# Optimization experiments

Measured on AMD Instinct MI355X. Metric: run time of the kernel, lower is better.

Reference implementation:

```python
import jax, jax.numpy as jnp
import numpy as np

# ---- dims / hyperparams (match init_kwargs) ----
D, B, S, NE, NC = 256, 4, 8192, 2048, 512
WIN, RK, TKE, TKC = 4, 4, 4, 4          # s window, route_topk, expanded_topk, compressed_topk
ALPHA, BS2B, BB2S = 1.0, 0.5, 0.5       # alpha_b, beta_s_to_b, beta_b_to_s
S_SC, B_SC, X_SC = 0.25, 0.2, 0.15      # s/b/cross delta scales
EPS = 1e-5
INV_SQRT_D = float(1.0 / np.sqrt(D))


def _ln(x, g, b):
    m = jnp.mean(x, -1, keepdims=True)
    v = jnp.mean(jnp.square(x - m), -1, keepdims=True)
    return (x - m) * jax.lax.rsqrt(v + EPS) * g + b


def _window_prop(state, val, w):
    # local window attention via diagonal-bilinear pairwise scores; never builds [S,S]
    n = state.shape[1]
    offs = jnp.arange(-WIN, WIN + 1)
    idx = jnp.arange(n)[:, None] + offs[None, :]            # [n, K]
    valid = (idx >= 0) & (idx < n)
    idxc = jnp.clip(idx, 0, n - 1)
    nb_s = state[:, idxc]                                    # [B, n, K, D]
    nb_v = val[:, idxc]
    sc = jnp.einsum('bnd,bnkd->bnk', state * w, nb_s) * INV_SQRT_D
    sc = jnp.where(valid, sc, -1e30)
    a = jax.nn.softmax(sc, axis=-1)
    return (jnp.einsum('bnk,bnkd->bnd', a, nb_s),
            jnp.einsum('bnk,bnkd->bnd', a, nb_v))


def _topk_prop(state, val, w, k):
    # global topk sparse attention over the (small) expanded/compressed node set
    sc = jnp.einsum('bnd,bmd->bnm', state * w, state) * INV_SQRT_D
    top, idx = jax.lax.top_k(sc, k)                          # [B, N, k]
    a = jax.nn.softmax(top, axis=-1)
    take = jax.vmap(lambda x, i: x[i])                       # gather rows per batch
    nb_s = take(state, idx)                                  # [B, N, k, D]
    nb_v = take(val, idx)
    return (jnp.einsum('bnk,bnkd->bnd', a, nb_s),
            jnp.einsum('bnk,bnkd->bnd', a, nb_v))


def _sparse_transition(src_s, src_v, W, bias, nd, k):
    # LinearRoute logits -> topk dst per src -> softmax weights -> scatter-add into dst
    logits = src_s @ W + bias                                # [B, Ns, Nd]
    top, idx = jax.lax.top_k(logits, k)
    wgt = jax.nn.softmax(top, axis=-1)                       # [B, Ns, k]

    def scat(i, ww, fs, fv):
        ii = i.reshape(-1)
        cs = (ww[..., None] * fs[:, None, :]).reshape(-1, fs.shape[-1])
        cv = (ww[..., None] * fv[:, None, :]).reshape(-1, fv.shape[-1])
        z = jnp.zeros((nd, fs.shape[-1]), fs.dtype)
        return z.at[ii].add(cs), z.at[ii].add(cv)

    return jax.vmap(scat)(idx, wgt, src_s, src_v)            # [B, Nd, D] x2


def _forward(s_state, s_val, w_pair_s, w_pair_e, w_pair_c,
             W_expand, b_expand, W_b2s, b_b2s, W_comp, b_comp, W_s2b, b_s2b,
             ln_g_s, ln_b_s, ln_g_e, ln_b_e, ln_g_c, ln_b_c):
    bsz = s_state.shape[0]
    # 1) sequence window propagation + stabilize
    ds, dv = _window_prop(s_state, s_val, w_pair_s)
    s_state = jnp.tanh(s_state + S_SC * ds)
    s_val = _ln(s_val + S_SC * dv, ln_g_s, ln_b_s)
    # 2) compressed layer bootstrapped from zeros (compressed_b=None) + stabilize
    c_state = jnp.zeros((bsz, NC, D), s_state.dtype)
    c_val = _ln(jnp.zeros((bsz, NC, D), s_state.dtype), ln_g_c, ln_b_c)
    # 3) expanded layer: expand transition then topk propagation + stabilize
    e_state = jnp.zeros((bsz, NE, D), s_state.dtype)
    e_val = jnp.zeros((bsz, NE, D), s_state.dtype)
    sc_b = ALPHA * B_SC
    ds, dv = _sparse_transition(c_state, c_val, W_expand, b_expand, NE, RK)
    e_state = e_state + sc_b * ds; e_val = e_val + sc_b * dv
    ds, dv = _topk_prop(e_state, e_val, w_pair_e, TKE)
    e_state = jnp.tanh(e_state + sc_b * ds)
    e_val = _ln(e_val + sc_b * dv, ln_g_e, ln_b_e)
    # 4) expanded -> sequence cross update + stabilize
    sc_x = ALPHA * BB2S * X_SC
    ds, dv = _sparse_transition(e_state, e_val, W_b2s, b_b2s, S, RK)
    s_state = jnp.tanh(s_state + sc_x * ds)
    s_val = _ln(s_val + sc_x * dv, ln_g_s, ln_b_s)
    # 5) next compressed: compress, s->b, compressed propagation + stabilize
    nc_state, nc_val = c_state, c_val
    ds, dv = _sparse_transition(e_state, e_val, W_comp, b_comp, NC, RK)
    nc_state = nc_state + sc_b * ds; nc_val = nc_val + sc_b * dv
    sc_sb = ALPHA * BS2B * X_SC
    ds, dv = _sparse_transition(s_state, s_val, W_s2b, b_s2b, NC, RK)
    nc_state = nc_state + sc_sb * ds; nc_val = nc_val + sc_sb * dv
    ds, dv = _topk_prop(nc_state, nc_val, w_pair_c, TKC)
    nc_state = jnp.tanh(nc_state + sc_b * ds)
    nc_val = _ln(nc_val + sc_b * dv, ln_g_c, ln_b_c)
    return (s_state, s_val, nc_state, nc_val)


def setup_inputs() -> dict:
    key = jax.random.key(0)
    ks = jax.random.split(key, 16)
    rs = float(1.0 / np.sqrt(D))
    return {
        's_state': jax.random.normal(ks[0], (B, S, D), jnp.float32),
        's_val': jax.random.normal(ks[1], (B, S, D), jnp.float32),
        'w_pair_s': jax.random.normal(ks[2], (D,), jnp.float32) * rs,
        'w_pair_e': jax.random.normal(ks[3], (D,), jnp.float32) * rs,
        'w_pair_c': jax.random.normal(ks[4], (D,), jnp.float32) * rs,
        'W_expand': jax.random.normal(ks[5], (D, NE), jnp.float32) * rs,
        'b_expand': jnp.zeros((NE,), jnp.float32),
        'W_b2s': jax.random.normal(ks[6], (D, S), jnp.float32) * rs,
        'b_b2s': jnp.zeros((S,), jnp.float32),
        'W_comp': jax.random.normal(ks[7], (D, NC), jnp.float32) * rs,
        'b_comp': jnp.zeros((NC,), jnp.float32),
        'W_s2b': jax.random.normal(ks[8], (D, NC), jnp.float32) * rs,
        'b_s2b': jnp.zeros((NC,), jnp.float32),
        'ln_g_s': jnp.ones((D,), jnp.float32), 'ln_b_s': jnp.zeros((D,), jnp.float32),
        'ln_g_e': jnp.ones((D,), jnp.float32), 'ln_b_e': jnp.zeros((D,), jnp.float32),
        'ln_g_c': jnp.ones((D,), jnp.float32), 'ln_b_c': jnp.zeros((D,), jnp.float32),
    }


def reference(s_state, s_val, w_pair_s, w_pair_e, w_pair_c,
              W_expand, b_expand, W_b2s, b_b2s, W_comp, b_comp, W_s2b, b_s2b,
              ln_g_s, ln_b_s, ln_g_e, ln_b_e, ln_g_c, ln_b_c):
    return _forward(s_state, s_val, w_pair_s, w_pair_e, w_pair_c,
                    W_expand, b_expand, W_b2s, b_b2s, W_comp, b_comp, W_s2b, b_s2b,
                    ln_g_s, ln_b_s, ln_g_e, ln_b_e, ln_g_c, ln_b_c)
```

## Files before the change

kernel.cpp:

```cpp
#include <hip/hip_runtime.h>
#include <math.h>

#define DD 256
#define BATCH 4
#define SEQ 8192
#define NEE 2048
#define NCC 512
#define EPSL 1e-5f
#define INV_SQRT_D 0.0625f

typedef __attribute__((ext_vector_type(8))) short short8;
typedef __attribute__((ext_vector_type(4))) float f32x4;

__device__ __forceinline__ float4 ld4(const float* p){ return *(const float4*)p; }
__device__ __forceinline__ void st4(float* p, const float4& v){ *(float4*)p = v; }
__device__ __forceinline__ void fma4(float4& a, float s, const float4& b){
  a.x = fmaf(s,b.x,a.x); a.y = fmaf(s,b.y,a.y); a.z = fmaf(s,b.z,a.z); a.w = fmaf(s,b.w,a.w);
}
__device__ __forceinline__ float4 tanh4(const float4& v){
  float4 r; r.x=tanhf(v.x); r.y=tanhf(v.y); r.z=tanhf(v.z); r.w=tanhf(v.w); return r;
}
__device__ __forceinline__ ushort f2bf(float x){
  unsigned u = __float_as_uint(x);
  unsigned r = u + 0x7fffu + ((u >> 16) & 1u);
  return (ushort)(r >> 16);
}
__device__ __forceinline__ float bf2f(ushort h){
  return __uint_as_float(((unsigned)h) << 16);
}

__device__ __forceinline__ bool t4_better(float v1, int i1, float v2, int i2){
  return (v1 > v2) || (v1 == v2 && i1 < i2);
}
__device__ __forceinline__ void t4_init(float* v, int* i){
#pragma unroll
  for (int k=0;k<4;k++){ v[k] = -INFINITY; i[k] = 0x7fffffff; }
}
__device__ __forceinline__ void t4_insert(float* v, int* i, float nv, int ni){
  if (t4_better(nv, ni, v[3], i[3])){
    v[3]=nv; i[3]=ni;
    if (t4_better(v[3],i[3],v[2],i[2])){ float tv=v[2]; v[2]=v[3]; v[3]=tv; int ti=i[2]; i[2]=i[3]; i[3]=ti;
      if (t4_better(v[2],i[2],v[1],i[1])){ tv=v[1]; v[1]=v[2]; v[2]=tv; ti=i[1]; i[1]=i[2]; i[2]=ti;
        if (t4_better(v[1],i[1],v[0],i[0])){ tv=v[0]; v[0]=v[1]; v[1]=tv; ti=i[0]; i[0]=i[1]; i[1]=ti; }
      }
    }
  }
}
__device__ __forceinline__ void t4_ce(float* v, int* i, int x, int y){
  if (t4_better(v[y],i[y],v[x],i[x])){ float tv=v[x]; v[x]=v[y]; v[y]=tv; int ti=i[x]; i[x]=i[y]; i[y]=ti; }
}
__device__ __forceinline__ void t4_merge(float* av, int* ai, const float* bv, const int* bi){
  float lv[4]; int li[4];
#pragma unroll
  for (int k=0;k<4;k++){
    if (t4_better(av[k],ai[k],bv[3-k],bi[3-k])){ lv[k]=av[k]; li[k]=ai[k]; }
    else { lv[k]=bv[3-k]; li[k]=bi[3-k]; }
  }
  t4_ce(lv,li,0,2); t4_ce(lv,li,1,3); t4_ce(lv,li,0,1); t4_ce(lv,li,2,3);
#pragma unroll
  for (int k=0;k<4;k++){ av[k]=lv[k]; ai[k]=li[k]; }
}
__device__ __forceinline__ void t4_wave_merge(float* v, int* i){
#pragma unroll
  for (int off=1; off<64; off<<=1){
    float bv[4]; int bi[4];
#pragma unroll
    for (int k=0;k<4;k++){ bv[k]=__shfl_xor(v[k],off); bi[k]=__shfl_xor(i[k],off); }
    t4_merge(v,i,bv,bi);
  }
}

__global__ __launch_bounds__(1024) void k0_prep(
    const float* __restrict__ b_expand, const float* __restrict__ b_b2s, const float* __restrict__ b_comp,
    const float* __restrict__ ln_b_c, const float* __restrict__ ln_g_e, const float* __restrict__ ln_b_e,
    float* __restrict__ sumE, int* __restrict__ idxB2S, float* __restrict__ wgtB2S,
    int* __restrict__ idxComp, float* __restrict__ wgtComp)
{
  __shared__ float wv_v[16][4];
  __shared__ int   wv_i[16][4];
  __shared__ int s_idx[3][4];
  __shared__ float s_wgt[3][4];
  __shared__ float red[16];
  int t = threadIdx.x, wv = t>>6, lane = t&63;
  {
    const float* arr; int n, base_wv, nw;
    if (wv < 2){ arr = b_expand; n = NEE; base_wv = 0;  nw = 2; }
    else if (wv < 14){ arr = b_b2s; n = SEQ; base_wv = 2; nw = 12; }
    else { arr = b_comp; n = NCC; base_wv = 14; nw = 2; }
    int gl = ((wv - base_wv)<<6) + lane;
    int stride = nw<<6;
    float v[4]; int ix[4]; t4_init(v,ix);
    for (int m=gl; m<n; m+=stride) t4_insert(v,ix, arr[m], m);
    t4_wave_merge(v,ix);
    if (lane==0){
#pragma unroll
      for (int k=0;k<4;k++){ wv_v[wv][k]=v[k]; wv_i[wv][k]=ix[k]; }
    }
  }
  __syncthreads();
  if (t < 3){
    int b0 = (t==0)? 0 : (t==1? 2 : 14);
    int nwv = (t==0)? 2 : (t==1? 12 : 2);
    float v[4]; int ix[4]; t4_init(v,ix);
    for (int wq=b0; wq<b0+nwv; wq++)
#pragma unroll
      for (int k=0;k<4;k++) t4_insert(v,ix, wv_v[wq][k], wv_i[wq][k]);
    float e0=1.f, e1=expf(v[1]-v[0]), e2=expf(v[2]-v[0]), e3=expf(v[3]-v[0]);
    float inv = 1.f/(e0+e1+e2+e3);
    s_idx[t][0]=ix[0]; s_idx[t][1]=ix[1]; s_idx[t][2]=ix[2]; s_idx[t][3]=ix[3];
    s_wgt[t][0]=e0*inv; s_wgt[t][1]=e1*inv; s_wgt[t][2]=e2*inv; s_wgt[t][3]=e3*inv;
  }
  __syncthreads();
  float c = (t < 256) ? ln_b_c[t] : 0.f;
  float cs = c, cq = c*c;
#pragma unroll
  for (int off=32; off; off>>=1){ cs += __shfl_xor(cs,off); cq += __shfl_xor(cq,off); }
  if (lane==0 && wv<4){ red[wv]=cs; red[8+wv]=cq; }
  __syncthreads();
  if (t < 256){
    float mean_c = (red[0]+red[1]+red[2]+red[3]) * (1.f/256.f);
    float var_c  = (red[8]+red[9]+red[10]+red[11]) * (1.f/256.f) - mean_c*mean_c;
    float cm = c - mean_c;
    float g = ln_g_e[t], be = ln_b_e[t];
    float a[4]; float q = 0.f;
#pragma unroll
    for (int k=0;k<4;k++){
      a[k] = 0.2f * (float)NCC * s_wgt[0][k];
      if (s_idx[0][k] < 4) q += a[k];
    }
    q *= 0.25f;
    float se = 0.f;
#pragma unroll
    for (int k=0;k<4;k++){
      float tk = a[k] + 0.2f*q;
      se += tk*cm*rsqrtf(tk*tk*var_c + EPSL)*g + be;
    }
    float tz = 0.2f*q;
    se += (float)(NEE-4) * (tz*cm*rsqrtf(tz*tz*var_c + EPSL)*g + be);
    sumE[t] = se;
    if (t < 4){
      idxB2S[t] = s_idx[1][t]; wgtB2S[t] = s_wgt[1][t];
      idxComp[t] = s_idx[2][t]; wgtComp[t] = s_wgt[2][t];
    }
  }
}

__global__ __launch_bounds__(256) void kz_init(int* __restrict__ counts,
    float* __restrict__ ncs, float* __restrict__ ncv,
    const float* __restrict__ ln_b_c, const float* __restrict__ sumE,
    const int* __restrict__ idxComp, const float* __restrict__ wgtComp)
{
  int bid = blockIdx.x;
  int t = threadIdx.x;
  if (bid < BATCH*NCC){
    int dest = bid & (NCC-1);
    float base = ln_b_c[t];
#pragma unroll
    for (int k=0;k<4;k++) if (dest == idxComp[k]) base = fmaf(0.2f*wgtComp[k], sumE[t], base);
    ncs[((size_t)bid<<8) + t] = 0.f;
    ncv[((size_t)bid<<8) + t] = base;
  } else {
    int i = (bid - BATCH*NCC)*256 + t;
    if (i < BATCH*NCC) counts[i] = 0;
  }
}

__global__ __launch_bounds__(256) void k1_window(
    const float* __restrict__ s_state, const float* __restrict__ s_val,
    const float* __restrict__ w_pair_s, const float* __restrict__ ln_g_s, const float* __restrict__ ln_b_s,
    const float* __restrict__ sumE, const int* __restrict__ idxB2S, const float* __restrict__ wgtB2S,
    float* __restrict__ out_state, float* __restrict__ out_val)
{
  int gw = (blockIdx.x << 2) + (threadIdx.x >> 6);
  int lane = threadIdx.x & 63;
  int b = gw >> 13, r = gw & (SEQ-1);
  size_t rowoff = ((size_t)gw) << 8;
  size_t bbase = ((size_t)b) << 21;
  int d0 = lane << 2;
  float4 x = ld4(s_state + rowoff + d0);
  float4 v = ld4(s_val + rowoff + d0);
  float4 wp = ld4(w_pair_s + d0);
  float qx=x.x*wp.x, qy=x.y*wp.y, qz=x.z*wp.z, qw=x.w*wp.w;
  float sc[9]; float4 ns[9];
#pragma unroll
  for (int k=0;k<9;k++){
    int rr = r + k - 4;
    int rc = rr < 0 ? 0 : (rr > SEQ-1 ? SEQ-1 : rr);
    ns[k] = ld4(s_state + bbase + (((size_t)rc)<<8) + d0);
    sc[k] = qx*ns[k].x + qy*ns[k].y + qz*ns[k].z + qw*ns[k].w;
  }
#pragma unroll
  for (int off=32; off; off>>=1){
#pragma unroll
    for (int k=0;k<9;k++) sc[k] += __shfl_xor(sc[k], off);
  }
  float mx = -INFINITY;
#pragma unroll
  for (int k=0;k<9;k++){
    int rr = r + k - 4;
    sc[k] = (rr>=0 && rr<SEQ) ? sc[k]*INV_SQRT_D : -1e30f;
    mx = fmaxf(mx, sc[k]);
  }
  float ssum = 0.f;
#pragma unroll
  for (int k=0;k<9;k++){ sc[k] = expf(sc[k]-mx); ssum += sc[k]; }
  float inv = 1.f/ssum;
  float4 ds = make_float4(0,0,0,0), dv = make_float4(0,0,0,0);
#pragma unroll
  for (int k=0;k<9;k++) fma4(ds, sc[k]*inv, ns[k]);
#pragma unroll
  for (int k=0;k<9;k++){
    int rr = r + k - 4;
    int rc = rr < 0 ? 0 : (rr > SEQ-1 ? SEQ-1 : rr);
    float4 nv = ld4(s_val + bbase + (((size_t)rc)<<8) + d0);
    fma4(dv, sc[k]*inv, nv);
  }
  float4 s1;
  s1.x = tanhf(x.x + 0.25f*ds.x); s1.y = tanhf(x.y + 0.25f*ds.y);
  s1.z = tanhf(x.z + 0.25f*ds.z); s1.w = tanhf(x.w + 0.25f*ds.w);
  st4(out_state + rowoff + d0, tanh4(s1));
  float4 y;
  y.x = v.x + 0.25f*dv.x; y.y = v.y + 0.25f*dv.y; y.z = v.z + 0.25f*dv.z; y.w = v.w + 0.25f*dv.w;
  float sm = y.x+y.y+y.z+y.w;
  float sq = y.x*y.x+y.y*y.y+y.z*y.z+y.w*y.w;
#pragma unroll
  for (int off=32; off; off>>=1){ sm += __shfl_xor(sm,off); sq += __shfl_xor(sq,off); }
  float mean = sm*(1.f/256.f);
  float rstd = rsqrtf(sq*(1.f/256.f) - mean*mean + EPSL);
  float4 g = ld4(ln_g_s + d0), be = ld4(ln_b_s + d0);
  float4 y1;
  y1.x = (y.x-mean)*rstd*g.x + be.x; y1.y = (y.y-mean)*rstd*g.y + be.y;
  y1.z = (y.z-mean)*rstd*g.z + be.z; y1.w = (y.w-mean)*rstd*g.w + be.w;
#pragma unroll
  for (int k=0;k<4;k++){
    if (r == idxB2S[k]){
      float cb = 0.075f * wgtB2S[k];
      float4 sE = ld4(sumE + d0);
      fma4(y1, cb, sE);
    }
  }
  sm = y1.x+y1.y+y1.z+y1.w;
  sq = y1.x*y1.x+y1.y*y1.y+y1.z*y1.z+y1.w*y1.w;
#pragma unroll
  for (int off=32; off; off>>=1){ sm += __shfl_xor(sm,off); sq += __shfl_xor(sq,off); }
  float mean2 = sm*(1.f/256.f);
  float rstd2 = rsqrtf(sq*(1.f/256.f) - mean2*mean2 + EPSL);
  float4 o;
  o.x = (y1.x-mean2)*rstd2*g.x + be.x; o.y = (y1.y-mean2)*rstd2*g.y + be.y;
  o.z = (y1.z-mean2)*rstd2*g.z + be.z; o.w = (y1.w-mean2)*rstd2*g.w + be.w;
  st4(out_val + rowoff + d0, o);
}

__global__ __launch_bounds__(256) void k2w_pack(const float* __restrict__ W,
    ushort* __restrict__ Whi, ushort* __restrict__ Wlo)
{
  int t = blockIdx.x*256 + threadIdx.x;
  int kb = t >> 11;
  int cf = (t >> 6) & 31;
  int l  = t & 63;
  int k0 = kb*32 + ((l>>4)<<3);
  int col = (cf<<4) + (l&15);
  size_t off = (size_t)t << 3;
#pragma unroll
  for (int j=0;j<8;j++){
    float x = W[(size_t)(k0+j)*NCC + col];
    ushort h = f2bf(x);
    Whi[off+j] = h;
    Wlo[off+j] = f2bf(x - bf2f(h));
  }
}

__global__ __launch_bounds__(256, 4) void k2_mfma(
    const float* __restrict__ A, const ushort* __restrict__ Whi,
    const float* __restrict__ bias,
    int* __restrict__ topk_idx, float* __restrict__ topk_wgt, int* __restrict__ counts)
{
  __shared__ __align__(16) ushort Asp[2][32][264];
  __shared__ float mv[32][17];
  __shared__ int   mi[32][17];
  int tid = threadIdx.x;
  size_t row_base = (size_t)blockIdx.x * 32;
  int w = tid >> 6, l = tid & 63;
  int lg = l >> 4, lr = l & 15;
  const ushort* pw = Whi + ((w<<12) + (l<<3));

#define LOADG(KB, G, DST) { \
    const ushort* _p = pw + (KB)*16384 + (G)*1024; \
    DST[0] = *(const short8*)_p; \
    DST[2] = *(const short8*)(_p + 512); \
    DST[1] = *(const short8*)(_p + 131072); \
    DST[3] = *(const short8*)(_p + 131072 + 512); }

#define COMPG(G, B) { \
    int _c0 = (G)<<1, _c1 = _c0+1; \
    acc[0][_c0] = __builtin_amdgcn_mfma_f32_16x16x32_bf16(ah0, B[0], acc[0][_c0], 0,0,0); \
    acc[1][_c0] = __builtin_amdgcn_mfma_f32_16x16x32_bf16(ah1, B[0], acc[1][_c0], 0,0,0); \
    acc[0][_c1] = __builtin_amdgcn_mfma_f32_16x16x32_bf16(ah0, B[2], acc[0][_c1], 0,0,0); \
    acc[1][_c1] = __builtin_amdgcn_mfma_f32_16x16x32_bf16(ah1, B[2], acc[1][_c1], 0,0,0); \
    acc[0][_c0] = __builtin_amdgcn_mfma_f32_16x16x32_bf16(al0, B[0], acc[0][_c0], 0,0,0); \
    acc[1][_c0] = __builtin_amdgcn_mfma_f32_16x16x32_bf16(al1, B[0], acc[1][_c0], 0,0,0); \
    acc[0][_c0] = __builtin_amdgcn_mfma_f32_16x16x32_bf16(ah0, B[1], acc[0][_c0], 0,0,0); \
    acc[1][_c0] = __builtin_amdgcn_mfma_f32_16x16x32_bf16(ah1, B[1], acc[1][_c0], 0,0,0); \
    acc[0][_c1] = __builtin_amdgcn_mfma_f32_16x16x32_bf16(al0, B[2], acc[0][_c1], 0,0,0); \
    acc[1][_c1] = __builtin_amdgcn_mfma_f32_16x16x32_bf16(al1, B[2], acc[1][_c1], 0,0,0); \
    acc[0][_c1] = __builtin_amdgcn_mfma_f32_16x16x32_bf16(ah0, B[3], acc[0][_c1], 0,0,0); \
    acc[1][_c1] = __builtin_amdgcn_mfma_f32_16x16x32_bf16(ah1, B[3], acc[1][_c1], 0,0,0); }

  short8 bA[4], bB[4];
  LOADG(0, 0, bA);
  {
    const float4* Ab = (const float4*)(A + row_base*DD);
#pragma unroll
    for (int i=0;i<8;i++){
      int q = i*256 + tid;
      int row = q >> 6, k4 = q & 63;
      float4 x = Ab[q];
      ushort4 h, lo;
      h.x = f2bf(x.x); h.y = f2bf(x.y); h.z = f2bf(x.z); h.w = f2bf(x.w);
      lo.x = f2bf(x.x - bf2f(h.x)); lo.y = f2bf(x.y - bf2f(h.y));
      lo.z = f2bf(x.z - bf2f(h.z)); lo.w = f2bf(x.w - bf2f(h.w));
      *(ushort4*)&Asp[0][row][k4*4] = h;
      *(ushort4*)&Asp[1][row][k4*4] = lo;
    }
  }
  __syncthreads();
  f32x4 acc[2][8];
#pragma unroll
  for (int rf=0; rf<2; rf++)
#pragma unroll
    for (int cf=0; cf<8; cf++) acc[rf][cf] = (f32x4){0.f,0.f,0.f,0.f};
#pragma unroll 1
  for (int kb=0; kb<8; kb++){
    int ka = kb*32 + (lg<<3);
    short8 ah0 = *(const short8*)&Asp[0][lr][ka];
    short8 ah1 = *(const short8*)&Asp[0][16+lr][ka];
    short8 al0 = *(const short8*)&Asp[1][lr][ka];
    short8 al1 = *(const short8*)&Asp[1][16+lr][ka];
    LOADG(kb, 1, bB);
    __builtin_amdgcn_sched_barrier(0);
    COMPG(0, bA);
    LOADG(kb, 2, bA);
    __builtin_amdgcn_sched_barrier(0);
    COMPG(1, bB);
    LOADG(kb, 3, bB);
    __builtin_amdgcn_sched_barrier(0);
    COMPG(2, bA);
    if (kb < 7) LOADG(kb+1, 0, bA);
    __builtin_amdgcn_sched_barrier(0);
    COMPG(3, bB);
  }
#undef LOADG
#undef COMPG
  float bcol[8];
  int rel[8];
#pragma unroll
  for (int cf=0; cf<8; cf++){
    bcol[cf] = bias[(w<<7) + (cf<<4) + lr];
    rel[cf] = (cf<<4) + lr;
  }
#pragma unroll
  for (int rf=0; rf<2; rf++){
#pragma unroll
    for (int reg=0; reg<4; reg++){
      float av[8];
#pragma unroll
      for (int cf=0; cf<8; cf++) av[cf] = acc[rf][cf][reg] + bcol[cf];
      float tv4[4]; int tc4[4];
#pragma unroll
      for (int r=0; r<4; r++){
        float m = fmaxf(fmaxf(fmaxf(av[0],av[1]),fmaxf(av[2],av[3])),
                        fmaxf(fmaxf(av[4],av[5]),fmaxf(av[6],av[7])));
#pragma unroll
        for (int off=1; off<16; off<<=1) m = fmaxf(m, __shfl_xor(m, off));
        int cand = 0x7fffffff;
#pragma unroll
        for (int cf=7; cf>=0; cf--) cand = (av[cf]==m) ? rel[cf] : cand;
#pragma unroll
        for (int off=1; off<16; off<<=1) cand = min(cand, __shfl_xor(cand, off));
        tv4[r] = m; tc4[r] = cand;
        if (r < 3){
#pragma unroll
          for (int cf=0; cf<8; cf++) av[cf] = (rel[cf]==cand) ? -INFINITY : av[cf];
        }
      }
      if (lr == 0){
        int rowl = (rf<<4) + (lg<<2) + reg;
#pragma unroll
        for (int r=0; r<4; r++){ mv[rowl][(w<<2)+r] = tv4[r]; mi[rowl][(w<<2)+r] = (w<<7) + tc4[r]; }
      }
    }
  }
  __syncthreads();
  if (tid < 32){
    float v[4]; int ix[4]; t4_init(v, ix);
#pragma unroll
    for (int j=0; j<16; j++) t4_insert(v, ix, mv[tid][j], mi[tid][j]);
    float e0=1.f, e1=expf(v[1]-v[0]), e2=expf(v[2]-v[0]), e3=expf(v[3]-v[0]);
    float inv = 1.f/(e0+e1+e2+e3);
    size_t row = row_base + tid;
    int b = (int)(row >> 13);
    topk_idx[row*4+0]=ix[0]; topk_idx[row*4+1]=ix[1]; topk_idx[row*4+2]=ix[2]; topk_idx[row*4+3]=ix[3];
    topk_wgt[row*4+0]=e0*inv; topk_wgt[row*4+1]=e1*inv; topk_wgt[row*4+2]=e2*inv; topk_wgt[row*4+3]=e3*inv;
    atomicAdd(&counts[(b<<9)+ix[0]],1); atomicAdd(&counts[(b<<9)+ix[1]],1);
    atomicAdd(&counts[(b<<9)+ix[2]],1); atomicAdd(&counts[(b<<9)+ix[3]],1);
  }
}

__global__ __launch_bounds__(256) void k3_scan(const int* __restrict__ counts,
    int* __restrict__ offsets, int* __restrict__ cursor)
{
  __shared__ int part[256];
  int t = threadIdx.x;
  int loc[8]; int s = 0;
#pragma unroll
  for (int i=0;i<8;i++){ loc[i] = counts[t*8+i]; s += loc[i]; }
  part[t] = s;
  __syncthreads();
  for (int off=1; off<256; off<<=1){
    int add = (t>=off)? part[t-off] : 0;
    __syncthreads();
    part[t] += add;
    __syncthreads();
  }
  int run = part[t] - s;
#pragma unroll
  for (int i=0;i<8;i++){ offsets[t*8+i] = run; cursor[t*8+i] = run; run += loc[i]; }
  if (t==255) offsets[BATCH*NCC] = run;
}

__global__ void k4_fill(const int* __restrict__ topk_idx, const float* __restrict__ topk_wgt,
    int* __restrict__ cursor, int* __restrict__ csr_src, float* __restrict__ csr_wgt)
{
  int row = blockIdx.x*256 + threadIdx.x;
  if (row >= BATCH*SEQ) return;
  int b = row >> 13, r = row & (SEQ-1);
#pragma unroll
  for (int k=0;k<4;k++){
    int dest = topk_idx[row*4+k];
    float wgt = topk_wgt[row*4+k];
    int pos = atomicAdd(&cursor[(b<<9)+dest], 1);
    csr_src[pos] = r;
    csr_wgt[pos] = 0.075f * wgt;
  }
}

__global__ __launch_bounds__(256) void k5_gather(
    const int* __restrict__ offsets, const int* __restrict__ csr_src, const float* __restrict__ csr_wgt,
    const float* __restrict__ st, const float* __restrict__ vl,
    float* __restrict__ ncs, float* __restrict__ ncv)
{
  int g2 = blockIdx.x;
  int g  = g2 >> 1;
  int half = g2 & 1;
  int b = g >> 9;
  int t = threadIdx.x;
  int i0 = offsets[g], i1 = offsets[g+1];
  int n = i1 - i0;
  int ia = i0 + ((n * half) >> 1);
  int ib = i0 + ((n * (half+1)) >> 1);
  if (ia >= ib) return;
  const float* Sb = st + (((size_t)b)<<21);
  const float* Vb = vl + (((size_t)b)<<21);
  float as0=0.f, as1=0.f, as2=0.f, as3=0.f;
  float av0=0.f, av1=0.f, av2=0.f, av3=0.f;
  int i = ia;
  for (; i+3 < ib; i += 4){
    int s0 = csr_src[i],   s1 = csr_src[i+1], s2 = csr_src[i+2], s3 = csr_src[i+3];
    float w0 = csr_wgt[i], w1 = csr_wgt[i+1], w2 = csr_wgt[i+2], w3 = csr_wgt[i+3];
    float x0 = Sb[((size_t)s0<<8)+t], y0 = Vb[((size_t)s0<<8)+t];
    float x1 = Sb[((size_t)s1<<8)+t], y1 = Vb[((size_t)s1<<8)+t];
    float x2 = Sb[((size_t)s2<<8)+t], y2 = Vb[((size_t)s2<<8)+t];
    float x3 = Sb[((size_t)s3<<8)+t], y3 = Vb[((size_t)s3<<8)+t];
    as0 = fmaf(w0,x0,as0); av0 = fmaf(w0,y0,av0);
    as1 = fmaf(w1,x1,as1); av1 = fmaf(w1,y1,av1);
    as2 = fmaf(w2,x2,as2); av2 = fmaf(w2,y2,av2);
    as3 = fmaf(w3,x3,as3); av3 = fmaf(w3,y3,av3);
  }
  for (; i < ib; i++){
    int src = csr_src[i];
    float wg = csr_wgt[i];
    as0 = fmaf(wg, Sb[((size_t)src<<8)+t], as0);
    av0 = fmaf(wg, Vb[((size_t)src<<8)+t], av0);
  }
  float accs = (as0+as1)+(as2+as3);
  float accv = (av0+av1)+(av2+av3);
  atomicAdd(&ncs[((size_t)g<<8) + t], accs);
  atomicAdd(&ncv[((size_t)g<<8) + t], accv);
}

__global__ __launch_bounds__(256) void k5t_transpose(const float* __restrict__ ncs, float* __restrict__ ncsT){
  __shared__ float tile[64][65];
  int b = blockIdx.z;
  int m0 = blockIdx.x*64, d0 = blockIdx.y*64;
  int tx = threadIdx.x & 63, ty = threadIdx.x >> 6;
  const float* src = ncs + (((size_t)b)<<17);
  for (int i=ty; i<64; i+=4) tile[i][tx] = src[(size_t)(m0+i)*DD + d0 + tx];
  __syncthreads();
  float* dst = ncsT + (((size_t)b)<<17);
  for (int i=ty; i<64; i+=4) dst[(size_t)(d0+i)*NCC + m0 + tx] = tile[tx][i];
}

__global__ __launch_bounds__(256) void k6_ncprop(
    const float* __restrict__ ncs, const float* __restrict__ ncv, const float* __restrict__ ncsT,
    const float* __restrict__ w_pair_c, const float* __restrict__ ln_g_c, const float* __restrict__ ln_b_c,
    float* __restrict__ o_ncs, float* __restrict__ o_ncv)
{
  __shared__ float Alds[256*13];
  int tid = threadIdx.x;
  int b = blockIdx.x >> 6;
  int n_base = (blockIdx.x & 63) << 3;
  const float* Sb = ncs + (((size_t)b)<<17);
  const float* Vb = ncv + (((size_t)b)<<17);
  const float* Tb = ncsT + (((size_t)b)<<17);
  float wc = w_pair_c[tid] * INV_SQRT_D;
#pragma unroll
  for (int i=0;i<8;i++) Alds[tid*13 + i] = Sb[(size_t)(n_base+i)*DD + tid] * wc;
  __syncthreads();
  int lane = tid & 63, rg = tid >> 6;
  int r0 = rg << 1, c0 = lane << 3;
  float acc[2][8];
#pragma unroll
  for (int j=0;j<2;j++)
#pragma unroll
    for (int c=0;c<8;c++) acc[j][c] = 0.f;
  for (int kk=0; kk<256; kk++){
    float4 w0 = ld4(Tb + (size_t)kk*NCC + c0);
    float4 w1 = ld4(Tb + (size_t)kk*NCC + c0 + 4);
    float a0 = Alds[kk*13 + r0];
    float a1 = Alds[kk*13 + r0 + 1];
    float wv_[8] = {w0.x,w0.y,w0.z,w0.w,w1.x,w1.y,w1.z,w1.w};
#pragma unroll
    for (int c=0;c<8;c++){
      acc[0][c] = fmaf(a0, wv_[c], acc[0][c]);
      acc[1][c] = fmaf(a1, wv_[c], acc[1][c]);
    }
  }
  int d0 = lane << 2;
  float4 g4 = ld4(ln_g_c + d0), be4 = ld4(ln_b_c + d0);
#pragma unroll
  for (int j=0;j<2;j++){
    float tv[4]; int ti[4]; t4_init(tv,ti);
#pragma unroll
    for (int c=0;c<8;c++) t4_insert(tv,ti, acc[j][c], c0+c);
    t4_wave_merge(tv,ti);
    float e0=1.f, e1=expf(tv[1]-tv[0]), e2=expf(tv[2]-tv[0]), e3=expf(tv[3]-tv[0]);
    float inv = 1.f/(e0+e1+e2+e3);
    float aw[4] = {e0*inv, e1*inv, e2*inv, e3*inv};
    int n = n_base + r0 + j;
    float4 stt = ld4(Sb + (size_t)n*DD + d0);
    float4 vv  = ld4(Vb + (size_t)n*DD + d0);
    float4 dsv = make_float4(0,0,0,0), dvv = make_float4(0,0,0,0);
#pragma unroll
    for (int k=0;k<4;k++){
      float4 ms = ld4(Sb + (size_t)ti[k]*DD + d0);
      float4 mv = ld4(Vb + (size_t)ti[k]*DD + d0);
      fma4(dsv, aw[k], ms); fma4(dvv, aw[k], mv);
    }
    float4 os;
    os.x = tanhf(stt.x + 0.2f*dsv.x); os.y = tanhf(stt.y + 0.2f*dsv.y);
    os.z = tanhf(stt.z + 0.2f*dsv.z); os.w = tanhf(stt.w + 0.2f*dsv.w);
    size_t orow = (((size_t)b)<<17) + ((size_t)n<<8);
    st4(o_ncs + orow + d0, os);
    float4 y;
    y.x = vv.x + 0.2f*dvv.x; y.y = vv.y + 0.2f*dvv.y;
    y.z = vv.z + 0.2f*dvv.z; y.w = vv.w + 0.2f*dvv.w;
    float sm = y.x+y.y+y.z+y.w;
    float sq = y.x*y.x+y.y*y.y+y.z*y.z+y.w*y.w;
#pragma unroll
    for (int off=32; off; off>>=1){ sm += __shfl_xor(sm,off); sq += __shfl_xor(sq,off); }
    float mean = sm*(1.f/256.f);
    float rstd = rsqrtf(sq*(1.f/256.f) - mean*mean + EPSL);
    float4 o;
    o.x = (y.x-mean)*rstd*g4.x + be4.x; o.y = (y.y-mean)*rstd*g4.y + be4.y;
    o.z = (y.z-mean)*rstd*g4.z + be4.z; o.w = (y.w-mean)*rstd*g4.w + be4.w;
    st4(o_ncv + orow + d0, o);
  }
}

extern "C" void kernel_launch(void* const* d_in, const int* in_sizes, int n_in,
                              void* d_out, int out_size, void* d_ws, size_t ws_size,
                              hipStream_t stream)
{
  const float* s_state = (const float*)d_in[0];
  const float* s_val   = (const float*)d_in[1];
  const float* w_pair_s= (const float*)d_in[2];
  const float* w_pair_c= (const float*)d_in[4];
  const float* b_expand= (const float*)d_in[6];
  const float* b_b2s   = (const float*)d_in[8];
  const float* b_comp  = (const float*)d_in[10];
  const float* W_s2b   = (const float*)d_in[11];
  const float* b_s2b   = (const float*)d_in[12];
  const float* ln_g_s  = (const float*)d_in[13];
  const float* ln_b_s  = (const float*)d_in[14];
  const float* ln_g_e  = (const float*)d_in[15];
  const float* ln_b_e  = (const float*)d_in[16];
  const float* ln_g_c  = (const float*)d_in[17];
  const float* ln_b_c  = (const float*)d_in[18];

  float* o_sstate = (float*)d_out;
  float* o_sval   = o_sstate + (size_t)BATCH*SEQ*DD;
  float* o_ncs    = o_sval + (size_t)BATCH*SEQ*DD;
  float* o_ncv    = o_ncs + (size_t)BATCH*NCC*DD;

  char* w = (char*)d_ws;
  float* sumE    = (float*)(w);
  int*   idxB2S  = (int*)(w + 1024);
  float* wgtB2S  = (float*)(w + 1040);
  int*   idxComp = (int*)(w + 1056);
  float* wgtComp = (float*)(w + 1072);
  int*   topk_idx= (int*)(w + 4096);
  float* topk_wgt= (float*)(w + 4096 + 524288);
  int*   counts  = (int*)(w + 1052672);
  int*   offsets = (int*)(w + 1069056);
  int*   cursor  = (int*)(w + 1085440);
  int*   csr_src = (int*)(w + 1101824);
  float* csr_wgt = (float*)(w + 1626112);
  float* ncs_ws  = (float*)(w + 2150400);
  float* ncv_ws  = ncs_ws + (size_t)BATCH*NCC*DD;
  float* ncsT_ws = ncv_ws + (size_t)BATCH*NCC*DD;
  ushort* wpk_hi = (ushort*)(w + 8441856);
  ushort* wpk_lo = (ushort*)(w + 8441856 + 262144);

  hipLaunchKernelGGL(k0_prep, dim3(1), dim3(1024), 0, stream,
      b_expand, b_b2s, b_comp, ln_b_c, ln_g_e, ln_b_e, sumE, idxB2S, wgtB2S, idxComp, wgtComp);
  hipLaunchKernelGGL(kz_init, dim3(BATCH*NCC + 8), dim3(256), 0, stream,
      counts, ncs_ws, ncv_ws, ln_b_c, sumE, idxComp, wgtComp);
  hipLaunchKernelGGL(k2w_pack, dim3(64), dim3(256), 0, stream, W_s2b, wpk_hi, wpk_lo);
  hipLaunchKernelGGL(k1_window, dim3(8192), dim3(256), 0, stream,
      s_state, s_val, w_pair_s, ln_g_s, ln_b_s, sumE, idxB2S, wgtB2S, o_sstate, o_sval);
  hipLaunchKernelGGL(k2_mfma, dim3(1024), dim3(256), 0, stream,
      o_sstate, wpk_hi, b_s2b, topk_idx, topk_wgt, counts);
  hipLaunchKernelGGL(k3_scan, dim3(1), dim3(256), 0, stream, counts, offsets, cursor);
  hipLaunchKernelGGL(k4_fill, dim3(128), dim3(256), 0, stream,
      topk_idx, topk_wgt, cursor, csr_src, csr_wgt);
  hipLaunchKernelGGL(k5_gather, dim3(4096), dim3(256), 0, stream,
      offsets, csr_src, csr_wgt, o_sstate, o_sval, ncs_ws, ncv_ws);
  hipLaunchKernelGGL(k5t_transpose, dim3(8,4,BATCH), dim3(256), 0, stream, ncs_ws, ncsT_ws);
  hipLaunchKernelGGL(k6_ncprop, dim3(256), dim3(256), 0, stream,
      ncs_ws, ncv_ws, ncsT_ws, w_pair_c, ln_g_c, ln_b_c, o_ncs, o_ncv);
}
```

Baseline: 361.0 us.

## Map window attention rows to 16-lane groups and use fast exp/tanh

The window-propagation kernel now processes one row per 16 threads instead of one per 64-lane wavefront, with each thread holding four float4 chunks. Launched blocks drop from 8192 to 2048. Cross-lane reductions shrink from 6 to 4 shuffle steps, and the work per shuffle rises. tanhf, expf and the division are replaced by __expf-based tanh and hardware reciprocal, which may lose accuracy and could overflow for large inputs.

```diff
diff --git a/kernel.cpp b/kernel.cpp
--- a/kernel.cpp
+++ b/kernel.cpp
@@ -19,6 +19,10 @@
 }
 __device__ __forceinline__ float4 tanh4(const float4& v){
   float4 r; r.x=tanhf(v.x); r.y=tanhf(v.y); r.z=tanhf(v.z); r.w=tanhf(v.w); return r;
+}
+__device__ __forceinline__ float tanh_e2(float x){
+  float z = __expf(2.f*x);
+  return (z - 1.f) * __builtin_amdgcn_rcpf(z + 1.f);
 }
 __device__ __forceinline__ ushort f2bf(float x){
   unsigned u = __float_as_uint(x);
@@ -171,26 +175,42 @@
     const float* __restrict__ sumE, const int* __restrict__ idxB2S, const float* __restrict__ wgtB2S,
     float* __restrict__ out_state, float* __restrict__ out_val)
 {
-  int gw = (blockIdx.x << 2) + (threadIdx.x >> 6);
-  int lane = threadIdx.x & 63;
-  int b = gw >> 13, r = gw & (SEQ-1);
-  size_t rowoff = ((size_t)gw) << 8;
+  int tid = threadIdx.x;
+  int li = tid & 15;
+  int grow = (blockIdx.x << 4) + (tid >> 4);
+  int b = grow >> 13, r = grow & (SEQ-1);
+  size_t rowoff = ((size_t)grow) << 8;
   size_t bbase = ((size_t)b) << 21;
-  int d0 = lane << 2;
-  float4 x = ld4(s_state + rowoff + d0);
-  float4 v = ld4(s_val + rowoff + d0);
-  float4 wp = ld4(w_pair_s + d0);
-  float qx=x.x*wp.x, qy=x.y*wp.y, qz=x.z*wp.z, qw=x.w*wp.w;
-  float sc[9]; float4 ns[9];
+  int e0 = li << 2;
+  int rcx[9];
 #pragma unroll
   for (int k=0;k<9;k++){
     int rr = r + k - 4;
-    int rc = rr < 0 ? 0 : (rr > SEQ-1 ? SEQ-1 : rr);
-    ns[k] = ld4(s_state + bbase + (((size_t)rc)<<8) + d0);
-    sc[k] = qx*ns[k].x + qy*ns[k].y + qz*ns[k].z + qw*ns[k].w;
-  }
-#pragma unroll
-  for (int off=32; off; off>>=1){
+    rcx[k] = rr < 0 ? 0 : (rr > SEQ-1 ? SEQ-1 : rr);
+  }
+  float4 x[4], v[4], q[4];
+#pragma unroll
+  for (int j=0;j<4;j++){
+    x[j] = ld4(s_state + rowoff + j*64 + e0);
+    v[j] = ld4(s_val + rowoff + j*64 + e0);
+    float4 wp = ld4(w_pair_s + j*64 + e0);
+    q[j].x = x[j].x*wp.x; q[j].y = x[j].y*wp.y; q[j].z = x[j].z*wp.z; q[j].w = x[j].w*wp.w;
+  }
+  float sc[9];
+#pragma unroll
+  for (int k=0;k<9;k++){
+    const float* ps = s_state + bbase + (((size_t)rcx[k])<<8) + e0;
+    float s = 0.f;
+#pragma unroll
+    for (int j=0;j<4;j++){
+      float4 n = ld4(ps + j*64);
+      s = fmaf(q[j].x, n.x, s); s = fmaf(q[j].y, n.y, s);
+      s = fmaf(q[j].z, n.z, s); s = fmaf(q[j].w, n.w, s);
+    }
+    sc[k] = s;
+  }
+#pragma unroll
+  for (int off=1; off<16; off<<=1){
 #pragma unroll
     for (int k=0;k<9;k++) sc[k] += __shfl_xor(sc[k], off);
   }
@@ -203,52 +223,88 @@
   }
   float ssum = 0.f;
 #pragma unroll
-  for (int k=0;k<9;k++){ sc[k] = expf(sc[k]-mx); ssum += sc[k]; }
-  float inv = 1.f/ssum;
-  float4 ds = make_float4(0,0,0,0), dv = make_float4(0,0,0,0);
-#pragma unroll
-  for (int k=0;k<9;k++) fma4(ds, sc[k]*inv, ns[k]);
+  for (int k=0;k<9;k++){ sc[k] = __expf(sc[k]-mx); ssum += sc[k]; }
+  float inv = __builtin_amdgcn_rcpf(ssum);
+#pragma unroll
+  for (int k=0;k<9;k++) sc[k] *= inv;
+  float4 ds[4], dv[4];
+#pragma unroll
+  for (int j=0;j<4;j++){ ds[j] = make_float4(0,0,0,0); dv[j] = make_float4(0,0,0,0); }
 #pragma unroll
   for (int k=0;k<9;k++){
-    int rr = r + k - 4;
-    int rc = rr < 0 ? 0 : (rr > SEQ-1 ? SEQ-1 : rr);
-    float4 nv = ld4(s_val + bbase + (((size_t)rc)<<8) + d0);
-    fma4(dv, sc[k]*inv, nv);
-  }
-  float4 s1;
-  s1.x = tanhf(x.x + 0.25f*ds.x); s1.y = tanhf(x.y + 0.25f*ds.y);
-  s1.z = tanhf(x.z + 0.25f*ds.z); s1.w = tanhf(x.w + 0.25f*ds.w);
-  st4(out_state + rowoff + d0, tanh4(s1));
-  float4 y;
-  y.x = v.x + 0.25f*dv.x; y.y = v.y + 0.25f*dv.y; y.z = v.z + 0.25f*dv.z; y.w = v.w + 0.25f*dv.w;
-  float sm = y.x+y.y+y.z+y.w;
-  float sq = y.x*y.x+y.y*y.y+y.z*y.z+y.w*y.w;
-#pragma unroll
-  for (int off=32; off; off>>=1){ sm += __shfl_xor(sm,off); sq += __shfl_xor(sq,off); }
+    float a = sc[k];
+    size_t nb = bbase + (((size_t)rcx[k])<<8) + e0;
+    const float* ps = s_state + nb;
+    const float* pv = s_val + nb;
+#pragma unroll
+    for (int j=0;j<4;j++){
+      float4 n = ld4(ps + j*64);
+      float4 m = ld4(pv + j*64);
+      fma4(ds[j], a, n); fma4(dv[j], a, m);
+    }
+  }
+#pragma unroll
+  for (int j=0;j<4;j++){
+    float4 s1;
+    s1.x = tanh_e2(x[j].x + 0.25f*ds[j].x); s1.y = tanh_e2(x[j].y + 0.25f*ds[j].y);
+    s1.z = tanh_e2(x[j].z + 0.25f*ds[j].z); s1.w = tanh_e2(x[j].w + 0.25f*ds[j].w);
+    float4 s2;
+    s2.x = tanh_e2(s1.x); s2.y = tanh_e2(s1.y); s2.z = tanh_e2(s1.z); s2.w = tanh_e2(s1.w);
+    st4(out_state + rowoff + j*64 + e0, s2);
+  }
+  float4 y[4];
+  float sm = 0.f, sq = 0.f;
+#pragma unroll
+  for (int j=0;j<4;j++){
+    y[j].x = v[j].x + 0.25f*dv[j].x; y[j].y = v[j].y + 0.25f*dv[j].y;
+    y[j].z = v[j].z + 0.25f*dv[j].z; y[j].w = v[j].w + 0.25f*dv[j].w;
+    sm += (y[j].x+y[j].y)+(y[j].z+y[j].w);
+    sq += (y[j].x*y[j].x+y[j].y*y[j].y)+(y[j].z*y[j].z+y[j].w*y[j].w);
+  }
+#pragma unroll
+  for (int off=1; off<16; off<<=1){ sm += __shfl_xor(sm,off); sq += __shfl_xor(sq,off); }
   float mean = sm*(1.f/256.f);
   float rstd = rsqrtf(sq*(1.f/256.f) - mean*mean + EPSL);
-  float4 g = ld4(ln_g_s + d0), be = ld4(ln_b_s + d0);
-  float4 y1;
-  y1.x = (y.x-mean)*rstd*g.x + be.x; y1.y = (y.y-mean)*rstd*g.y + be.y;
-  y1.z = (y.z-mean)*rstd*g.z + be.z; y1.w = (y.w-mean)*rstd*g.w + be.w;
+  float4 g[4], be[4];
+#pragma unroll
+  for (int j=0;j<4;j++){
+    g[j] = ld4(ln_g_s + j*64 + e0);
+    be[j] = ld4(ln_b_s + j*64 + e0);
+    y[j].x = (y[j].x-mean)*rstd*g[j].x + be[j].x;
+    y[j].y = (y[j].y-mean)*rstd*g[j].y + be[j].y;
+    y[j].z = (y[j].z-mean)*rstd*g[j].z + be[j].z;
+    y[j].w = (y[j].w-mean)*rstd*g[j].w + be[j].w;
+  }
 #pragma unroll
   for (int k=0;k<4;k++){
     if (r == idxB2S[k]){
       float cb = 0.075f * wgtB2S[k];
-      float4 sE = ld4(sumE + d0);
-      fma4(y1, cb, sE);
-    }
-  }
-  sm = y1.x+y1.y+y1.z+y1.w;
-  sq = y1.x*y1.x+y1.y*y1.y+y1.z*y1.z+y1.w*y1.w;
-#pragma unroll
-  for (int off=32; off; off>>=1){ sm += __shfl_xor(sm,off); sq += __shfl_xor(sq,off); }
+#pragma unroll
+      for (int j=0;j<4;j++){
+        float4 sE = ld4(sumE + j*64 + e0);
+        fma4(y[j], cb, sE);
+      }
+    }
+  }
+  sm = 0.f; sq = 0.f;
+#pragma unroll
+  for (int j=0;j<4;j++){
+    sm += (y[j].x+y[j].y)+(y[j].z+y[j].w);
+    sq += (y[j].x*y[j].x+y[j].y*y[j].y)+(y[j].z*y[j].z+y[j].w*y[j].w);
+  }
+#pragma unroll
+  for (int off=1; off<16; off<<=1){ sm += __shfl_xor(sm,off); sq += __shfl_xor(sq,off); }
   float mean2 = sm*(1.f/256.f);
   float rstd2 = rsqrtf(sq*(1.f/256.f) - mean2*mean2 + EPSL);
-  float4 o;
-  o.x = (y1.x-mean2)*rstd2*g.x + be.x; o.y = (y1.y-mean2)*rstd2*g.y + be.y;
-  o.z = (y1.z-mean2)*rstd2*g.z + be.z; o.w = (y1.w-mean2)*rstd2*g.w + be.w;
-  st4(out_val + rowoff + d0, o);
+#pragma unroll
+  for (int j=0;j<4;j++){
+    float4 o;
+    o.x = (y[j].x-mean2)*rstd2*g[j].x + be[j].x;
+    o.y = (y[j].y-mean2)*rstd2*g[j].y + be[j].y;
+    o.z = (y[j].z-mean2)*rstd2*g[j].z + be[j].z;
+    o.w = (y[j].w-mean2)*rstd2*g[j].w + be[j].w;
+    st4(out_val + rowoff + j*64 + e0, o);
+  }
 }
 
 __global__ __launch_bounds__(256) void k2w_pack(const float* __restrict__ W,
@@ -626,7 +682,7 @@
   hipLaunchKernelGGL(kz_init, dim3(BATCH*NCC + 8), dim3(256), 0, stream,
       counts, ncs_ws, ncv_ws, ln_b_c, sumE, idxComp, wgtComp);
   hipLaunchKernelGGL(k2w_pack, dim3(64), dim3(256), 0, stream, W_s2b, wpk_hi, wpk_lo);
-  hipLaunchKernelGGL(k1_window, dim3(8192), dim3(256), 0, stream,
+  hipLaunchKernelGGL(k1_window, dim3(2048), dim3(256), 0, stream,
       s_state, s_val, w_pair_s, ln_g_s, ln_b_s, sumE, idxB2S, wgtB2S, o_sstate, o_sval);
   hipLaunchKernelGGL(k2_mfma, dim3(1024), dim3(256), 0, stream,
       o_sstate, wpk_hi, b_s2b, topk_idx, topk_wgt, counts);
```

Result: slower. 488.3 us (+35.3%).
